# Optimization experiments

Hardware: AMD Instinct MI355X
Metric: run time of the kernel (lower is better)

Reference implementation:

```python
import jax, jax.numpy as jnp
import numpy as np

B, N, Th, Td, Tw, Tp = 8, 3000, 24, 12, 24, 12
T2a, T2b, K = 64, 32, 3  # hidden temporal dims of the two STBlocks, Cheb order


def _laplacian(A):
    # PyG ChebConv with lambda_max=None -> lambda_max=2.0, sym normalization:
    # L_hat = 2L/lambda_max - I = -D^{-1/2} A D^{-1/2} with zero diagonal
    Aod = A * (1.0 - jnp.eye(A.shape[0], dtype=A.dtype))
    deg = Aod.sum(axis=1)
    dinv = jnp.where(deg > 0, deg ** -0.5, 0.0)
    return -(dinv[:, None] * Aod * dinv[None, :])


def _cheb(x, L, W, b):
    # Chebyshev graph conv, K=3. x: (B,N,Cin), L: (N,N), W: (K,Cin,Cout), b: (Cout,)
    Tx0 = x
    Tx1 = jnp.einsum('nm,bmi->bni', L, Tx0)
    Tx2 = 2.0 * jnp.einsum('nm,bmi->bni', L, Tx1) - Tx0
    out = (jnp.einsum('bni,io->bno', Tx0, W[0])
           + jnp.einsum('bni,io->bno', Tx1, W[1])
           + jnp.einsum('bni,io->bno', Tx2, W[2]))
    return out + b


def _tconv(x, w, b):
    # Conv1d(1, 1, 3, padding=1) over last axis. x: (B,N,T), w: (3,), b: scalar
    xp = jnp.pad(x, ((0, 0), (0, 0), (1, 1)))
    return w[0] * xp[..., :-2] + w[1] * xp[..., 1:-1] + w[2] * xp[..., 2:] + b


def _stblock(x, L, W, bg, cw, cb):
    x = jax.nn.relu(_cheb(x, L, W, bg))
    return jax.nn.relu(_tconv(x, cw, cb))


def _branch(X, L, W1, b1, c1w, c1b, W2, b2, c2w, c2b, WD, bD):
    x = X.reshape(X.shape[0], X.shape[1], X.shape[3])  # (B,N,T)
    x = _stblock(x, L, W1, b1, c1w, c1b)  # (B,N,64)
    x = _stblock(x, L, W2, b2, c2w, c2b)  # (B,N,32)
    return jax.nn.relu(x @ WD + bD)       # (B,N,Tp); forward only uses LinearD


def setup_inputs() -> dict:
    ks = jax.random.split(jax.random.key(0), 48)
    it = iter(range(48))

    def nrm(shape, s=1.0):
        return jax.random.normal(ks[next(it)], shape, jnp.float32) * s

    Xh = nrm((B, N, 1, Th))
    Xd = nrm((B, N, 1, Td))
    Xw = nrm((B, N, 1, Tw))
    u = jax.random.uniform(ks[next(it)], (N, N))
    w = jax.random.uniform(ks[next(it)], (N, N))
    A = jnp.where(u < 0.01, w, 0.0)
    A = 0.5 * (A + A.T)

    def gcn_p(ti, to):
        return nrm((K, ti, to), (2.0 / (ti + to)) ** 0.5), jnp.zeros((to,), jnp.float32)

    def conv_p():
        return nrm((K,), 0.4), nrm((), 0.1)

    Wh1, bh1 = gcn_p(Th, T2a); ch1w, ch1b = conv_p()
    Wh2, bh2 = gcn_p(T2a, T2b); ch2w, ch2b = conv_p()
    Wd1, bd1 = gcn_p(Td, T2a); cd1w, cd1b = conv_p()
    Wd2, bd2 = gcn_p(T2a, T2b); cd2w, cd2b = conv_p()
    Ww1, bw1 = gcn_p(Tw, T2a); cw1w, cw1b = conv_p()
    Ww2, bw2 = gcn_p(T2a, T2b); cw2w, cw2b = conv_p()
    WD = nrm((T2b, Tp), (2.0 / (T2b + Tp)) ** 0.5)
    bD = jnp.zeros((Tp,), jnp.float32)
    Fh = jax.random.uniform(ks[next(it)], (Tp,), jnp.float32)
    Fd = jax.random.uniform(ks[next(it)], (Tp,), jnp.float32)
    Fw = jax.random.uniform(ks[next(it)], (Tp,), jnp.float32)

    return dict(Xh=Xh, Xd=Xd, Xw=Xw, A=A,
                Wh1=Wh1, bh1=bh1, ch1w=ch1w, ch1b=ch1b, Wh2=Wh2, bh2=bh2, ch2w=ch2w, ch2b=ch2b,
                Wd1=Wd1, bd1=bd1, cd1w=cd1w, cd1b=cd1b, Wd2=Wd2, bd2=bd2, cd2w=cd2w, cd2b=cd2b,
                Ww1=Ww1, bw1=bw1, cw1w=cw1w, cw1b=cw1b, Ww2=Ww2, bw2=bw2, cw2w=cw2w, cw2b=cw2b,
                WD=WD, bD=bD, Fh=Fh, Fd=Fd, Fw=Fw)


def reference(Xh, Xd, Xw, A,
              Wh1, bh1, ch1w, ch1b, Wh2, bh2, ch2w, ch2b,
              Wd1, bd1, cd1w, cd1b, Wd2, bd2, cd2w, cd2b,
              Ww1, bw1, cw1w, cw1b, Ww2, bw2, cw2w, cw2b,
              WD, bD, Fh, Fd, Fw):
    L = _laplacian(A)
    Yh = _branch(Xh, L, Wh1, bh1, ch1w, ch1b, Wh2, bh2, ch2w, ch2b, WD, bD)
    Yd = _branch(Xd, L, Wd1, bd1, cd1w, cd1b, Wd2, bd2, cd2w, cd2b, WD, bD)
    Yw = _branch(Xw, L, Ww1, bw1, cw1w, cw1b, Ww2, bw2, cw2w, cw2b, WD, bD)
    Y = Fh * Yh + Fd * Yd + Fw * Yw  # Fusion: elementwise weighted sum over Tp
    return Y[:, :, None, :]  # (B,N,1,Tp)
```

## Files before the change

kernel.cpp:

```cpp
#include <hip/hip_runtime.h>

#define NN 3000
#define NB 8
#define TP 12
#define DMAX 128
#define F1T 480
#define F2T 768

struct BrW {
    const float *W1[3]; const float *b1[3]; const float *c1w[3]; const float *c1b[3];
    const float *W2[3]; const float *b2[3]; const float *c2w[3]; const float *c2b[3];
    const float *Fb[3];
};

__global__ void build_kernel(const float* __restrict__ A, int* __restrict__ colp,
                             float* __restrict__ valp, int* __restrict__ cnt,
                             float* __restrict__ dinv) {
    int n = blockIdx.x;
    int lane = threadIdx.x;
    const float4* row4 = reinterpret_cast<const float4*>(A + (size_t)n * NN);
    int base = 0;
    float s = 0.f;
    for (int start = 0; start < 750; start += 64) {
        int m4 = start + lane;
        float4 v = make_float4(0.f, 0.f, 0.f, 0.f);
        if (m4 < 750) v = row4[m4];
        float vals[4] = {v.x, v.y, v.z, v.w};
        int mbase = m4 * 4;
        #pragma unroll
        for (int u = 0; u < 4; ++u) {
            int m = mbase + u;
            float a = (m4 < 750 && m != n) ? vals[u] : 0.f;
            bool nz = (a != 0.f);
            s += a;
            unsigned long long mask = __ballot(nz);
            int off = __popcll(mask & ((1ull << lane) - 1ull));
            if (nz) {
                int idx = base + off;
                if (idx < DMAX) { colp[n * DMAX + idx] = m; valp[n * DMAX + idx] = a; }
            }
            base += __popcll(mask);
        }
    }
    for (int o = 32; o > 0; o >>= 1) s += __shfl_down(s, o);
    if (lane == 0) {
        cnt[n] = (base < DMAX) ? base : DMAX;
        dinv[n] = (s > 0.f) ? 1.0f / sqrtf(s) : 0.f;
    }
}

__global__ void scale_pack_kernel(const int* __restrict__ colp, float* __restrict__ valp,
                                  const int* __restrict__ cnt, const float* __restrict__ dinv,
                                  const float* __restrict__ Xh, const float* __restrict__ Xd,
                                  const float* __restrict__ Xw, float* __restrict__ xcat) {
    int bid = blockIdx.x;
    if (bid < NN) {
        int n = bid;
        int j = threadIdx.x;
        if (j < DMAX && j < cnt[n]) {
            int m = colp[n * DMAX + j];
            valp[n * DMAX + j] *= -dinv[n] * dinv[m];
        }
    } else {
        int idx = (bid - NN) * 256 + threadIdx.x;
        if (idx >= NN * F1T) return;
        int n = idx / F1T, r = idx % F1T;
        const float* src; int b, t, T;
        if (r < 192)      { src = Xh; T = 24; int rr = r;       b = rr / 24; t = rr % 24; }
        else if (r < 288) { src = Xd; T = 12; int rr = r - 192; b = rr / 12; t = rr % 12; }
        else              { src = Xw; T = 24; int rr = r - 288; b = rr / 24; t = rr % 24; }
        xcat[idx] = src[((size_t)b * NN + n) * T + t];
    }
}

template <int F, int SLICE, int EPI>
__global__ void spmm_kernel(const int* __restrict__ colp, const float* __restrict__ valp,
                            const int* __restrict__ cnt, const float* __restrict__ x,
                            const float* __restrict__ aux, float* __restrict__ y) {
    int nwg = gridDim.x;
    int q = nwg >> 3;
    int bid = blockIdx.x;
    int w = (bid & 7) * q + (bid >> 3);
    int slice = w / NN;
    int n = w - slice * NN;
    int f = slice * SLICE + threadIdx.x;

    __shared__ int   scol[DMAX];
    __shared__ float sval[DMAX];
    int c = cnt[n];
    if (threadIdx.x < DMAX) {
        int j = threadIdx.x;
        bool ok = j < c;
        scol[j] = ok ? colp[n * DMAX + j] * F : 0;
        sval[j] = ok ? valp[n * DMAX + j] : 0.f;
    }
    __syncthreads();
    int c32 = (c + 31) & ~31;
    float a0 = 0.f, a1 = 0.f, a2 = 0.f, a3 = 0.f;
    float a4 = 0.f, a5 = 0.f, a6 = 0.f, a7 = 0.f;
    if (f < F) {
        for (int i = 0; i < c32; i += 32) {
            float g[32], w32[32];
            #pragma unroll
            for (int u = 0; u < 32; ++u) {
                int cc = scol[i + u];
                w32[u] = sval[i + u];
                g[u] = x[cc + f];
            }
            #pragma unroll
            for (int u = 0; u < 32; u += 8) {
                a0 += w32[u + 0] * g[u + 0]; a1 += w32[u + 1] * g[u + 1];
                a2 += w32[u + 2] * g[u + 2]; a3 += w32[u + 3] * g[u + 3];
                a4 += w32[u + 4] * g[u + 4]; a5 += w32[u + 5] * g[u + 5];
                a6 += w32[u + 6] * g[u + 6]; a7 += w32[u + 7] * g[u + 7];
            }
        }
    }
    if (f >= F) return;
    float acc = ((a0 + a1) + (a2 + a3)) + ((a4 + a5) + (a6 + a7));
    size_t o = (size_t)n * F + f;
    if (EPI == 1) acc = 2.f * acc - aux[o];
    else if (EPI == 2) acc = aux[o] + 2.f * acc;
    y[o] = acc;
}

#define SZ_LDA 67
template <int T, int OFF>
__device__ __forceinline__ void fused1_body(
        int tile, int br, const float* __restrict__ xcat, const float* __restrict__ t1cat,
        const float* __restrict__ t2cat, float* __restrict__ y1cat,
        float* __restrict__ y2cat, float* __restrict__ c0cat, const BrW& P, float* smem) {
    constexpr int K = 3 * T;
    constexpr int LDA = K + 1;
    int tid = threadIdx.x;
    float* sW1 = smem;
    float* sX  = smem + K * 64;
    const float* W1 = P.W1[br];
    for (int i = tid; i < K * 64; i += 192) sW1[i] = W1[i];
    int n0 = tile * 12;
    #pragma unroll
    for (int s = 0; s < 3; ++s) {
        const float* src = (s == 0) ? xcat : (s == 1) ? t1cat : t2cat;
        for (int i = tid; i < 96 * T; i += 192) {
            int n_l = i / (8 * T), rem = i % (8 * T);
            int b = rem / T, ii = rem % T;
            sX[(n_l * 8 + b) * LDA + s * T + ii] =
                src[(size_t)(n0 + n_l) * F1T + OFF + b * T + ii];
        }
    }
    __syncthreads();

    int rq = tid >> 3;
    int g  = tid & 7;
    float acc[4][8];
    #pragma unroll
    for (int r = 0; r < 4; ++r)
        #pragma unroll
        for (int j = 0; j < 8; ++j) acc[r][j] = 0.f;

    #pragma unroll 4
    for (int k = 0; k < K; ++k) {
        const float4* wr = reinterpret_cast<const float4*>(sW1 + k * 64 + g * 8);
        float4 wa = wr[0], wb = wr[1];
        #pragma unroll
        for (int r = 0; r < 4; ++r) {
            float zv = sX[(rq * 4 + r) * LDA + k];
            acc[r][0] += zv * wa.x; acc[r][1] += zv * wa.y;
            acc[r][2] += zv * wa.z; acc[r][3] += zv * wa.w;
            acc[r][4] += zv * wb.x; acc[r][5] += zv * wb.y;
            acc[r][6] += zv * wb.z; acc[r][7] += zv * wb.w;
        }
    }

    float bgv[8];
    #pragma unroll
    for (int j = 0; j < 8; ++j) bgv[j] = P.b1[br][g * 8 + j];
    float w0 = P.c1w[br][0], w1 = P.c1w[br][1], w2 = P.c1w[br][2], bb = P.c1b[br][0];

    float o[4][8];
    #pragma unroll
    for (int r = 0; r < 4; ++r) {
        float z[8];
        #pragma unroll
        for (int j = 0; j < 8; ++j) z[j] = fmaxf(acc[r][j] + bgv[j], 0.f);
        float zl = __shfl_up(z[7], 1);
        float zr = __shfl_down(z[0], 1);
        #pragma unroll
        for (int j = 0; j < 8; ++j) {
            float left  = (j > 0) ? z[j - 1] : ((g > 0) ? zl : 0.f);
            float right = (j < 7) ? z[j + 1] : ((g < 7) ? zr : 0.f);
            o[r][j] = fmaxf(w0 * left + w1 * z[j] + w2 * right + bb, 0.f);
        }
    }
    __syncthreads();

    float* sZ  = smem;
    float* sW2 = smem + 96 * SZ_LDA;
    #pragma unroll
    for (int r = 0; r < 4; ++r) {
        float* dst = sZ + (rq * 4 + r) * SZ_LDA + g * 8;
        #pragma unroll
        for (int j = 0; j < 8; ++j) dst[j] = o[r][j];
    }
    const float* W2 = P.W2[br];
    for (int i = tid; i < 6144; i += 192) {
        int k = i / 96, cc = i % 96;
        int j = cc / 3, m = cc % 3;
        sW2[i] = W2[m * 2048 + k * 32 + j];
    }
    __syncthreads();

    float acc2[4][12];
    #pragma unroll
    for (int r = 0; r < 4; ++r)
        #pragma unroll
        for (int j = 0; j < 12; ++j) acc2[r][j] = 0.f;

    #pragma unroll 4
    for (int k = 0; k < 64; ++k) {
        const float4* wr = reinterpret_cast<const float4*>(sW2 + k * 96 + g * 12);
        float4 wa = wr[0], wb = wr[1], wc = wr[2];
        #pragma unroll
        for (int r = 0; r < 4; ++r) {
            float zv = sZ[(rq * 4 + r) * SZ_LDA + k];
            acc2[r][0] += zv * wa.x;  acc2[r][1] += zv * wa.y;
            acc2[r][2] += zv * wa.z;  acc2[r][3] += zv * wa.w;
            acc2[r][4] += zv * wb.x;  acc2[r][5] += zv * wb.y;
            acc2[r][6] += zv * wb.z;  acc2[r][7] += zv * wb.w;
            acc2[r][8] += zv * wc.x;  acc2[r][9] += zv * wc.y;
            acc2[r][10] += zv * wc.z; acc2[r][11] += zv * wc.w;
        }
    }

    const float* b2 = P.b2[br];
    #pragma unroll
    for (int r = 0; r < 4; ++r) {
        int unit = tile * 96 + rq * 4 + r;
        int n = unit >> 3, b = unit & 7;
        size_t obase = (size_t)n * F2T + br * 256 + b * 32;
        #pragma unroll
        for (int jj = 0; jj < 4; ++jj) {
            int j = g * 4 + jj;
            float a0 = acc2[r][jj * 3 + 0], a1 = acc2[r][jj * 3 + 1], a2 = acc2[r][jj * 3 + 2];
            y1cat[obase + j] = a1;
            y2cat[obase + j] = a2;
            c0cat[obase + j] = a0 - a2 + b2[j];
        }
    }
}

__global__ void __launch_bounds__(192, 2)
fused1_kernel(const float* __restrict__ xcat, const float* __restrict__ t1cat,
              const float* __restrict__ t2cat, float* __restrict__ y1cat,
              float* __restrict__ y2cat, float* __restrict__ c0cat, BrW P) {
    __shared__ float smem[12576];
    int b = blockIdx.x;
    if (b < 250)      fused1_body<24, 0>(b, 0, xcat, t1cat, t2cat, y1cat, y2cat, c0cat, P, smem);
    else if (b < 500) fused1_body<12, 192>(b - 250, 1, xcat, t1cat, t2cat, y1cat, y2cat, c0cat, P, smem);
    else              fused1_body<24, 288>(b - 500, 2, xcat, t1cat, t2cat, y1cat, y2cat, c0cat, P, smem);
}

__global__ void __launch_bounds__(768)
spmm_final_kernel(const int* __restrict__ colp, const float* __restrict__ valp,
                  const int* __restrict__ cnt, const float* __restrict__ x,
                  const float* __restrict__ c0cat, const float* __restrict__ WD,
                  const float* __restrict__ bD, float* __restrict__ out, BrW P) {
    int bid = blockIdx.x;
    int n = (bid & 7) * (NN / 8) + (bid >> 3);
    int f = threadIdx.x;

    __shared__ int   scol[DMAX];
    __shared__ float sval[DMAX];
    __shared__ float z2[3][NB][32];
    int c = cnt[n];
    if (threadIdx.x < DMAX) {
        int j = threadIdx.x;
        bool ok = j < c;
        scol[j] = ok ? colp[n * DMAX + j] * F2T : 0;
        sval[j] = ok ? valp[n * DMAX + j] : 0.f;
    }
    __syncthreads();
    int c32 = (c + 31) & ~31;
    float a0 = 0.f, a1 = 0.f, a2 = 0.f, a3 = 0.f;
    float a4 = 0.f, a5 = 0.f, a6 = 0.f, a7 = 0.f;
    for (int i = 0; i < c32; i += 32) {
        float g[32], w32[32];
        #pragma unroll
        for (int u = 0; u < 32; ++u) {
            int cc = scol[i + u];
            w32[u] = sval[i + u];
            g[u] = x[cc + f];
        }
        #pragma unroll
        for (int u = 0; u < 32; u += 8) {
            a0 += w32[u + 0] * g[u + 0]; a1 += w32[u + 1] * g[u + 1];
            a2 += w32[u + 2] * g[u + 2]; a3 += w32[u + 3] * g[u + 3];
            a4 += w32[u + 4] * g[u + 4]; a5 += w32[u + 5] * g[u + 5];
            a6 += w32[u + 6] * g[u + 6]; a7 += w32[u + 7] * g[u + 7];
        }
    }
    float v = ((a0 + a1) + (a2 + a3)) + ((a4 + a5) + (a6 + a7));

    int co = f & 31;
    int unit = f >> 5;
    int br = unit >> 3, b = unit & 7;
    float a = fmaxf(c0cat[(size_t)n * F2T + f] + v, 0.f);
    float left  = __shfl_up(a, 1);
    float right = __shfl_down(a, 1);
    if (co == 0) left = 0.f;
    if (co == 31) right = 0.f;
    float w0 = P.c2w[br][0], w1 = P.c2w[br][1], w2 = P.c2w[br][2], bb = P.c2b[br][0];
    z2[br][b][co] = fmaxf(w0 * left + w1 * a + w2 * right + bb, 0.f);
    __syncthreads();

    if (threadIdx.x < NB * TP) {
        int b2 = threadIdx.x / TP, tp = threadIdx.x % TP;
        float y = 0.f;
        for (int brr = 0; brr < 3; ++brr) {
            float s = bD[tp];
            const float* zz = z2[brr][b2];
            for (int cc = 0; cc < 32; ++cc) s += zz[cc] * WD[cc * TP + tp];
            y += fmaxf(s, 0.f) * P.Fb[brr][tp];
        }
        out[((size_t)b2 * NN + n) * TP + tp] = y;
    }
}


static inline size_t align256(size_t x) { return (x + 255) & ~(size_t)255; }

extern "C" void kernel_launch(void* const* d_in, const int* in_sizes, int n_in,
                              void* d_out, int out_size, void* d_ws, size_t ws_size,
                              hipStream_t stream) {
    const float* Xh = (const float*)d_in[0];
    const float* Xd = (const float*)d_in[1];
    const float* Xw = (const float*)d_in[2];
    const float* A  = (const float*)d_in[3];
    const float* WD = (const float*)d_in[28];
    const float* bD = (const float*)d_in[29];

    BrW P;
    for (int br = 0; br < 3; ++br) {
        int base = 4 + br * 8;
        P.W1[br]  = (const float*)d_in[base + 0];
        P.b1[br]  = (const float*)d_in[base + 1];
        P.c1w[br] = (const float*)d_in[base + 2];
        P.c1b[br] = (const float*)d_in[base + 3];
        P.W2[br]  = (const float*)d_in[base + 4];
        P.b2[br]  = (const float*)d_in[base + 5];
        P.c2w[br] = (const float*)d_in[base + 6];
        P.c2b[br] = (const float*)d_in[base + 7];
        P.Fb[br]  = (const float*)d_in[30 + br];
    }

    char* p = (char*)d_ws;
    int*   colp  = (int*)p;   p += align256((size_t)NN * DMAX * 4);
    float* valp  = (float*)p; p += align256((size_t)NN * DMAX * 4);
    int*   cnt   = (int*)p;   p += align256(NN * 4);
    float* dinv  = (float*)p; p += align256(NN * 4);
    float* xcat  = (float*)p; p += align256((size_t)NN * F1T * 4);
    float* t1cat = (float*)p; p += align256((size_t)NN * F1T * 4);
    float* t2cat = (float*)p; p += align256((size_t)NN * F1T * 4);
    float* y1cat = (float*)p; p += align256((size_t)NN * F2T * 4);
    float* y2cat = (float*)p; p += align256((size_t)NN * F2T * 4);
    float* c0cat = (float*)p; p += align256((size_t)NN * F2T * 4);
    float* scat  = (float*)p; p += align256((size_t)NN * F2T * 4);

    build_kernel<<<NN, 64, 0, stream>>>(A, colp, valp, cnt, dinv);
    scale_pack_kernel<<<NN + (NN * F1T + 255) / 256, 256, 0, stream>>>(
        colp, valp, cnt, dinv, Xh, Xd, Xw, xcat);

    spmm_kernel<F1T, 256, 0><<<6000, 256, 0, stream>>>(colp, valp, cnt, xcat, nullptr, t1cat);
    spmm_kernel<F1T, 256, 1><<<6000, 256, 0, stream>>>(colp, valp, cnt, t1cat, xcat, t2cat);

    fused1_kernel<<<750, 192, 0, stream>>>(xcat, t1cat, t2cat, y1cat, y2cat, c0cat, P);

    spmm_kernel<F2T, 128, 2><<<18000, 128, 0, stream>>>(colp, valp, cnt, y2cat, y1cat, scat);
    spmm_final_kernel<<<NN, 768, 0, stream>>>(colp, valp, cnt, scat, c0cat, WD, bD,
                                              (float*)d_out, P);
}
```

Measured before the change: 195.1 us.

## Split final SpMM into generic spmm kernel plus lightweight combine kernel

Replaces the fused final SpMM-plus-epilogue kernel (one 768-thread block per node) with the generic 128-thread spmm_kernel over 18000 blocks, writing to a new vcat buffer. A separate combine kernel then adds c0cat, applies the temporal conv, and does the dense output projection. The aim is better parallelism and occupancy for the gather. The cost is an extra launch and an extra round trip of an N×768 intermediate through memory.

```diff
diff --git a/kernel.cpp b/kernel.cpp
--- a/kernel.cpp
+++ b/kernel.cpp
@@ -260,51 +260,17 @@
     else              fused1_body<24, 288>(b - 500, 2, xcat, t1cat, t2cat, y1cat, y2cat, c0cat, P, smem);
 }
 
-__global__ void __launch_bounds__(768)
-spmm_final_kernel(const int* __restrict__ colp, const float* __restrict__ valp,
-                  const int* __restrict__ cnt, const float* __restrict__ x,
-                  const float* __restrict__ c0cat, const float* __restrict__ WD,
-                  const float* __restrict__ bD, float* __restrict__ out, BrW P) {
-    int bid = blockIdx.x;
-    int n = (bid & 7) * (NN / 8) + (bid >> 3);
-    int f = threadIdx.x;
-
-    __shared__ int   scol[DMAX];
-    __shared__ float sval[DMAX];
+__global__ void combine2_final_kernel(const float* __restrict__ c0cat,
+                                      const float* __restrict__ vcat,
+                                      const float* __restrict__ WD, const float* __restrict__ bD,
+                                      float* __restrict__ out, BrW P) {
+    int n = blockIdx.x;
     __shared__ float z2[3][NB][32];
-    int c = cnt[n];
-    if (threadIdx.x < DMAX) {
-        int j = threadIdx.x;
-        bool ok = j < c;
-        scol[j] = ok ? colp[n * DMAX + j] * F2T : 0;
-        sval[j] = ok ? valp[n * DMAX + j] : 0.f;
-    }
-    __syncthreads();
-    int c32 = (c + 31) & ~31;
-    float a0 = 0.f, a1 = 0.f, a2 = 0.f, a3 = 0.f;
-    float a4 = 0.f, a5 = 0.f, a6 = 0.f, a7 = 0.f;
-    for (int i = 0; i < c32; i += 32) {
-        float g[32], w32[32];
-        #pragma unroll
-        for (int u = 0; u < 32; ++u) {
-            int cc = scol[i + u];
-            w32[u] = sval[i + u];
-            g[u] = x[cc + f];
-        }
-        #pragma unroll
-        for (int u = 0; u < 32; u += 8) {
-            a0 += w32[u + 0] * g[u + 0]; a1 += w32[u + 1] * g[u + 1];
-            a2 += w32[u + 2] * g[u + 2]; a3 += w32[u + 3] * g[u + 3];
-            a4 += w32[u + 4] * g[u + 4]; a5 += w32[u + 5] * g[u + 5];
-            a6 += w32[u + 6] * g[u + 6]; a7 += w32[u + 7] * g[u + 7];
-        }
-    }
-    float v = ((a0 + a1) + (a2 + a3)) + ((a4 + a5) + (a6 + a7));
-
-    int co = f & 31;
-    int unit = f >> 5;
+    int unit = threadIdx.x >> 5;
+    int co = threadIdx.x & 31;
     int br = unit >> 3, b = unit & 7;
-    float a = fmaxf(c0cat[(size_t)n * F2T + f] + v, 0.f);
+    size_t o = (size_t)n * F2T + br * 256 + b * 32 + co;
+    float a = fmaxf(c0cat[o] + vcat[o], 0.f);
     float left  = __shfl_up(a, 1);
     float right = __shfl_down(a, 1);
     if (co == 0) left = 0.f;
@@ -312,14 +278,13 @@
     float w0 = P.c2w[br][0], w1 = P.c2w[br][1], w2 = P.c2w[br][2], bb = P.c2b[br][0];
     z2[br][b][co] = fmaxf(w0 * left + w1 * a + w2 * right + bb, 0.f);
     __syncthreads();
-
     if (threadIdx.x < NB * TP) {
         int b2 = threadIdx.x / TP, tp = threadIdx.x % TP;
         float y = 0.f;
         for (int brr = 0; brr < 3; ++brr) {
             float s = bD[tp];
             const float* zz = z2[brr][b2];
-            for (int cc = 0; cc < 32; ++cc) s += zz[cc] * WD[cc * TP + tp];
+            for (int c = 0; c < 32; ++c) s += zz[c] * WD[c * TP + tp];
             y += fmaxf(s, 0.f) * P.Fb[brr][tp];
         }
         out[((size_t)b2 * NN + n) * TP + tp] = y;
@@ -365,6 +330,7 @@
     float* y2cat = (float*)p; p += align256((size_t)NN * F2T * 4);
     float* c0cat = (float*)p; p += align256((size_t)NN * F2T * 4);
     float* scat  = (float*)p; p += align256((size_t)NN * F2T * 4);
+    float* vcat  = (float*)p; p += align256((size_t)NN * F2T * 4);
 
     build_kernel<<<NN, 64, 0, stream>>>(A, colp, valp, cnt, dinv);
     scale_pack_kernel<<<NN + (NN * F1T + 255) / 256, 256, 0, stream>>>(
@@ -376,6 +342,7 @@
     fused1_kernel<<<750, 192, 0, stream>>>(xcat, t1cat, t2cat, y1cat, y2cat, c0cat, P);
 
     spmm_kernel<F2T, 128, 2><<<18000, 128, 0, stream>>>(colp, valp, cnt, y2cat, y1cat, scat);
-    spmm_final_kernel<<<NN, 768, 0, stream>>>(colp, valp, cnt, scat, c0cat, WD, bD,
-                                              (float*)d_out, P);
-}
+    spmm_kernel<F2T, 128, 0><<<18000, 128, 0, stream>>>(colp, valp, cnt, scat, nullptr, vcat);
+
+    combine2_final_kernel<<<NN, 768, 0, stream>>>(c0cat, vcat, WD, bD, (float*)d_out, P);
+}
```

Result: faster. 170.1 us (-12.8%).
